# Kernel optimization log

Hardware: AMD Instinct MI355X
Metric: run time of the kernel (lower is better)

Reference implementation:

```python
import jax, jax.numpy as jnp
import numpy as np

B, S, D, H = 4, 2048, 1024, 16
HD = D // H  # head_dim = 64

def setup_inputs() -> dict:
    key = jax.random.key(0)
    ks = jax.random.split(key, 5)
    scale = 1.0 / np.sqrt(D)
    return {
        "x": jax.random.normal(ks[0], (B, S, D), dtype=jnp.float32),
        "Wqkv": jax.random.normal(ks[1], (D, 3 * D), dtype=jnp.float32) * scale,
        "bqkv": jax.random.normal(ks[2], (3 * D,), dtype=jnp.float32) * 0.01,
        "Wo": jax.random.normal(ks[3], (D, D), dtype=jnp.float32) * scale,
        "bo": jax.random.normal(ks[4], (D,), dtype=jnp.float32) * 0.01,
    }

def reference(x, Wqkv, bqkv, Wo, bo):
    b, s, d = x.shape
    # fused QKV projection: [B,S,3D]
    qkv = jnp.einsum("bsd,de->bse", x, Wqkv) + bqkv
    # [B,S,H,3*HD] -> [B,H,S,3*HD], then chunk into q,k,v per head
    qkv = qkv.reshape(b, s, H, 3 * HD).transpose(0, 2, 1, 3)
    q, k, v = jnp.split(qkv, 3, axis=-1)  # each [B,H,S,HD]
    inv_sqrt_dk = jnp.asarray(1.0 / np.sqrt(HD), dtype=x.dtype)
    scores = jnp.einsum("bhqd,bhkd->bhqk", q, k) * inv_sqrt_dk
    attn = jax.nn.softmax(scores, axis=-1)
    values = jnp.einsum("bhqk,bhkd->bhqd", attn, v)  # [B,H,S,HD]
    # NOTE: source reshapes [B,H,S,HD] -> [B,S,H*HD] WITHOUT permuting back
    # (a quirk of the original code); replicated faithfully.
    values = values.reshape(b, s, d)
    out = jnp.einsum("bsd,de->bse", values, Wo) + bo
    return out
```

## Files before the change

### kernel.cpp

```cpp
#include <hip/hip_runtime.h>
#include <hip/hip_bf16.h>
#include <cstdint>

static constexpr int Bq  = 4;
static constexpr int Sq  = 2048;
static constexpr int Dq  = 1024;
static constexpr int Hq  = 16;
static constexpr int HDq = 64;
static constexpr int ROWS = Bq * Sq;
static constexpr int QKV_N = 3 * Dq;

typedef __bf16 bf16x8 __attribute__((ext_vector_type(8)));
typedef __bf16 bf16x4 __attribute__((ext_vector_type(4)));
typedef __bf16 bf16x2 __attribute__((ext_vector_type(2)));
typedef float  floatx4 __attribute__((ext_vector_type(4)));
typedef float  floatx16 __attribute__((ext_vector_type(16)));
typedef unsigned int uintx4 __attribute__((ext_vector_type(4)));

#define MFMA16(a, b, c) __builtin_amdgcn_mfma_f32_16x16x32_bf16((a), (b), (c), 0, 0, 0)
#define MFMA32(a, b, c) __builtin_amdgcn_mfma_f32_32x32x16_bf16((a), (b), (c), 0, 0, 0)

#define QSCALE 0.18033688011112042f

__device__ __forceinline__ void async16(const void* g, void* l) {
    __builtin_amdgcn_global_load_lds(
        (const __attribute__((address_space(1))) uint32_t*)g,
        (__attribute__((address_space(3))) uint32_t*)l, 16, 0, 0);
}

__global__ __launch_bounds__(256) void cvt4_kernel(const float4* __restrict__ in,
                                                   bf16x4* __restrict__ out, int n4) {
    int i = blockIdx.x * 256 + threadIdx.x;
    if (i < n4) {
        float4 v = in[i];
        bf16x4 o;
        o[0] = (__bf16)v.x; o[1] = (__bf16)v.y; o[2] = (__bf16)v.z; o[3] = (__bf16)v.w;
        out[i] = o;
    }
}

__global__ __launch_bounds__(256) void tcvt_kernel(const float* __restrict__ in,
                                                   __bf16* __restrict__ out, int K, int N) {
    __shared__ float t[32][33];
    int n0 = blockIdx.x * 32, k0 = blockIdx.y * 32;
    int c = threadIdx.x & 31, r0 = threadIdx.x >> 5;
#pragma unroll
    for (int rr = 0; rr < 32; rr += 8)
        t[r0 + rr][c] = in[(size_t)(k0 + r0 + rr) * N + n0 + c];
    __syncthreads();
#pragma unroll
    for (int rr = 0; rr < 32; rr += 8)
        out[(size_t)(n0 + r0 + rr) * K + k0 + c] = (__bf16)t[c][r0 + rr];
}

template <int MODE>
__global__ __launch_bounds__(256) void gemm_bt_kernel(const __bf16* __restrict__ A,
                                                      const __bf16* __restrict__ BT,
                                                      const float* __restrict__ bias,
                                                      void* __restrict__ Cout,
                                                      __bf16* __restrict__ Vt,
                                                      int M, int N, int K) {
    __shared__ __bf16 As[128 * 32];
    __shared__ __bf16 Bs[128 * 32];

    const int t = threadIdx.x;
    const int lane = t & 63;
    const int wave = t >> 6;
    const int wm = wave & 1, wn = wave >> 1;
    const int l15 = lane & 15;
    const int kg = (lane >> 4) * 8;

    const int m0 = blockIdx.y * 128;
    const int n0 = blockIdx.x * 128;

    const int srow = t >> 2;
    const int scol = (t & 3) * 8;
    const __bf16* ag = A  + (size_t)(m0 + srow) * K + scol;
    const __bf16* bg = BT + (size_t)(n0 + srow) * K + scol;
    __bf16* al = As + t * 8;
    __bf16* bl = Bs + t * 8;

    floatx4 acc[4][4] = {};

    for (int k0 = 0; k0 < K; k0 += 32) {
        __syncthreads();
        async16(ag + k0,                    al);
        async16(ag + (size_t)64 * K + k0,   al + 2048);
        async16(bg + k0,                    bl);
        async16(bg + (size_t)64 * K + k0,   bl + 2048);
        __syncthreads();

        bf16x8 af[4], bfr[4];
#pragma unroll
        for (int mi = 0; mi < 4; ++mi)
            af[mi] = *(const bf16x8*)(As + (wm * 64 + mi * 16 + l15) * 32 + kg);
#pragma unroll
        for (int ni = 0; ni < 4; ++ni)
            bfr[ni] = *(const bf16x8*)(Bs + (wn * 64 + ni * 16 + l15) * 32 + kg);
#pragma unroll
        for (int mi = 0; mi < 4; ++mi)
#pragma unroll
            for (int ni = 0; ni < 4; ++ni)
                acc[mi][ni] = MFMA16(af[mi], bfr[ni], acc[mi][ni]);
    }

    const int r0 = (lane >> 4) * 4;
    const int wn0 = n0 + wn * 64;

    if (MODE == 2 && (wn0 % 192) == 128) {
#pragma unroll
        for (int ni = 0; ni < 4; ++ni) {
            int col = wn0 + ni * 16 + l15;
            float bv = bias[col];
            int h = col / 192;
            int d = col - h * 192 - 128;
#pragma unroll
            for (int mi = 0; mi < 4; ++mi) {
                int row = m0 + wm * 64 + mi * 16 + r0;
                int b = row >> 11, s = row & 2047;
                bf16x4 vv;
#pragma unroll
                for (int i = 0; i < 4; ++i) vv[i] = (__bf16)(acc[mi][ni][i] + bv);
                *(bf16x4*)(Vt + ((size_t)(b * Hq + h) * HDq + d) * Sq + s) = vv;
            }
        }
    } else {
        const float sc = (MODE == 2 && (wn0 % 192) == 0) ? QSCALE : 1.0f;
#pragma unroll
        for (int ni = 0; ni < 4; ++ni) {
            int col = wn0 + ni * 16 + l15;
            float bv = bias[col];
#pragma unroll
            for (int mi = 0; mi < 4; ++mi) {
#pragma unroll
                for (int i = 0; i < 4; ++i) {
                    int row = m0 + wm * 64 + mi * 16 + r0 + i;
                    float v = (acc[mi][ni][i] + bv) * sc;
                    size_t off = (size_t)row * N + col;
                    if (MODE == 1) ((float*)Cout)[off] = v;
                    else           ((__bf16*)Cout)[off] = (__bf16)v;
                }
            }
        }
    }
}

__global__ __launch_bounds__(256, 2) void attn_kernel(const __bf16* __restrict__ qkv,
                                                      const __bf16* __restrict__ Vt,
                                                      __bf16* __restrict__ v2) {
    const int bh = blockIdx.x;
    const int b = bh >> 4, h = bh & 15;
    const int q0 = blockIdx.y * 256;
    const int tid  = threadIdx.x;
    const int lane = tid & 63;
    const int wave = tid >> 6;
    const int l31  = lane & 31;
    const int hi   = lane >> 5;
    const int kx   = l31 & 7;
    const size_t rs = QKV_N;
    const __bf16* base  = qkv + (size_t)b * Sq * rs + (size_t)h * (3 * HDq);
    const __bf16* vbase = Vt + (size_t)bh * HDq * Sq;

    __shared__ alignas(16) __bf16 Ks[2][64][64];
    __shared__ alignas(16) __bf16 Vs[2][64][64];

    bf16x8 qb[2][4];
#pragma unroll
    for (int qg = 0; qg < 2; ++qg) {
        const __bf16* qr = base + (size_t)(q0 + wave * 64 + qg * 32 + l31) * rs + hi * 8;
#pragma unroll
        for (int st = 0; st < 4; ++st) qb[qg][st] = *(const bf16x8*)(qr + st * 16);
    }

    const int rA = wave * 8 + (lane >> 3);
    const int rB = rA + 32;
    const int sw = ((lane & 7) ^ (rA & 7)) * 8;
    const __bf16* gK0 = base + HDq + (size_t)rA * rs + sw;
    const __bf16* gK1 = base + HDq + (size_t)rB * rs + sw;
    const __bf16* gV0 = vbase + (size_t)rA * Sq + sw;
    const __bf16* gV1 = vbase + (size_t)rB * Sq + sw;
    const int loff0 = wave * 512 + lane * 8;
    const int loff1 = (4 + wave) * 512 + lane * 8;

    auto STAGE = [&](int bufi, int kt) {
        const size_t ko = (size_t)kt * rs;
        async16(gK0 + ko, &Ks[bufi][0][0] + loff0);
        async16(gK1 + ko, &Ks[bufi][0][0] + loff1);
        async16(gV0 + kt, &Vs[bufi][0][0] + loff0);
        async16(gV1 + kt, &Vs[bufi][0][0] + loff1);
    };

    auto softmax_pb = [&](const floatx16& c, float& la, bf16x8* pb) {
        unsigned int W[8];
        float s0 = 0.f, s1 = 0.f;
#pragma unroll
        for (int m = 0; m < 8; ++m) {
            float e0 = __builtin_amdgcn_exp2f(c[2 * m]);
            float e1 = __builtin_amdgcn_exp2f(c[2 * m + 1]);
            s0 += e0; s1 += e1;
            union { bf16x2 v; unsigned int u; } pk;
            pk.v[0] = (__bf16)e0; pk.v[1] = (__bf16)e1;
            W[m] = pk.u;
        }
        la += s0 + s1;
#pragma unroll
        for (int ks = 0; ks < 2; ++ks) {
            auto r0 = __builtin_amdgcn_permlane32_swap(W[ks * 4 + 0], W[ks * 4 + 2], false, false);
            auto r1 = __builtin_amdgcn_permlane32_swap(W[ks * 4 + 1], W[ks * 4 + 3], false, false);
            uintx4 bb; bb[0] = r0[0]; bb[1] = r1[0]; bb[2] = r0[1]; bb[3] = r1[1];
            pb[ks] = __builtin_bit_cast(bf16x8, bb);
        }
    };

    floatx16 o[2][2] = {};
    float la0 = 0.f, la1 = 0.f;

    STAGE(0, 0);
    __syncthreads();

    int cur = 0;
    for (int kt = 0; kt < Sq; kt += 64, cur ^= 1) {
        if (kt + 64 < Sq) STAGE(cur ^ 1, kt + 64);

#pragma unroll
        for (int half = 0; half < 2; ++half) {
            const int key = half * 32 + l31;

            floatx16 c0 = {}, c1 = {};
#pragma unroll
            for (int st = 0; st < 4; ++st) {
                bf16x8 a = *(const bf16x8*)(&Ks[cur][key][((st * 2 + hi) ^ kx) * 8]);
                c0 = MFMA32(a, qb[0][st], c0);
                c1 = MFMA32(a, qb[1][st], c1);
            }

            bf16x8 pb0[2], pb1[2];
            softmax_pb(c0, la0, pb0);
            softmax_pb(c1, la1, pb1);

#pragma unroll
            for (int ks = 0; ks < 2; ++ks) {
                const int kslot = half * 4 + ks * 2 + hi;
                bf16x8 va0 = *(const bf16x8*)(&Vs[cur][l31][(kslot ^ kx) * 8]);
                bf16x8 va1 = *(const bf16x8*)(&Vs[cur][32 + l31][(kslot ^ kx) * 8]);
                o[0][0] = MFMA32(va0, pb0[ks], o[0][0]);
                o[0][1] = MFMA32(va1, pb0[ks], o[0][1]);
                o[1][0] = MFMA32(va0, pb1[ks], o[1][0]);
                o[1][1] = MFMA32(va1, pb1[ks], o[1][1]);
            }
        }
        __syncthreads();
    }

#pragma unroll
    for (int qg = 0; qg < 2; ++qg) {
        float lsum = qg ? la1 : la0;
        float l = lsum + __shfl_xor(lsum, 32);
        float rinv = 1.0f / l;
        const int q = q0 + wave * 64 + qg * 32 + l31;
        size_t row = (size_t)b * Sq + h * 128 + (q >> 4);
        __bf16* vrow = v2 + row * Dq + (size_t)(q & 15) * 64;
#pragma unroll
        for (int gg = 0; gg < 4; ++gg) {
            bf16x4 ov;
#pragma unroll
            for (int i = 0; i < 4; ++i) ov[i] = (__bf16)(o[qg][0][gg * 4 + i] * rinv);
            *(bf16x4*)(vrow + gg * 8 + hi * 4) = ov;
#pragma unroll
            for (int i = 0; i < 4; ++i) ov[i] = (__bf16)(o[qg][1][gg * 4 + i] * rinv);
            *(bf16x4*)(vrow + 32 + gg * 8 + hi * 4) = ov;
        }
    }
}

extern "C" void kernel_launch(void* const* d_in, const int* in_sizes, int n_in,
                              void* d_out, int out_size, void* d_ws, size_t ws_size,
                              hipStream_t stream) {
    const float* x    = (const float*)d_in[0];
    const float* Wqkv = (const float*)d_in[1];
    const float* bqkv = (const float*)d_in[2];
    const float* Wo   = (const float*)d_in[3];
    const float* bo   = (const float*)d_in[4];
    float* out = (float*)d_out;

    __bf16* xb    = (__bf16*)d_ws;
    __bf16* WqkvT = xb    + (size_t)ROWS * Dq;
    __bf16* WoT   = WqkvT + (size_t)QKV_N * Dq;
    __bf16* qkvb  = WoT   + (size_t)Dq * Dq;
    __bf16* Vt    = qkvb  + (size_t)ROWS * QKV_N;
    __bf16* v2    = xb;

    const int nx4 = ROWS * Dq / 4;
    cvt4_kernel<<<(nx4 + 255) / 256, 256, 0, stream>>>((const float4*)x, (bf16x4*)xb, nx4);
    tcvt_kernel<<<dim3(QKV_N / 32, Dq / 32), 256, 0, stream>>>(Wqkv, WqkvT, Dq, QKV_N);
    tcvt_kernel<<<dim3(Dq / 32, Dq / 32), 256, 0, stream>>>(Wo, WoT, Dq, Dq);

    gemm_bt_kernel<2><<<dim3(QKV_N / 128, ROWS / 128), 256, 0, stream>>>(
        xb, WqkvT, bqkv, (void*)qkvb, Vt, ROWS, QKV_N, Dq);

    attn_kernel<<<dim3(Bq * Hq, Sq / 256), 256, 0, stream>>>(qkvb, Vt, v2);

    gemm_bt_kernel<1><<<dim3(Dq / 128, ROWS / 128), 256, 0, stream>>>(
        v2, WoT, bo, (void*)out, nullptr, ROWS, Dq, Dq);
}
```

Baseline: 278.6 us.

## Add dedicated 256x256 QKV GEMM with async double-buffered LDS pipeline

Replaces the generic 128x128 QKV projection GEMM with a specialized 512-thread kernel. It uses 256x256 tiles, 32x32x16 MFMA, XOR-swizzled LDS, async global-to-LDS loads double-buffered across K steps, and interleaves loads with compute phases using barriers and setprio. The goal is higher MFMA utilization and better latency hiding for the largest GEMM. The generic kernel is reduced to the output-projection path only. Costs include larger LDS and register use, and a hand-tuned vmcnt schedule that is fragile.

After: 282.5 us. Within noise of the previous version (+1.4%).

```diff
diff --git a/kernel.cpp b/kernel.cpp
--- a/kernel.cpp
+++ b/kernel.cpp
@@ -51,6 +51,158 @@
 #pragma unroll
     for (int rr = 0; rr < 32; rr += 8)
         out[(size_t)(n0 + r0 + rr) * K + k0 + c] = (__bf16)t[c][r0 + rr];
+}
+
+__global__ __launch_bounds__(512, 2) void gemm_qkv_kernel(const __bf16* __restrict__ A,
+                                                          const __bf16* __restrict__ BT,
+                                                          const float* __restrict__ bias,
+                                                          __bf16* __restrict__ qkvb,
+                                                          __bf16* __restrict__ Vt) {
+    __shared__ __bf16 lds[2][2][2][128][64];
+
+    const int tid  = threadIdx.x;
+    const int lane = tid & 63;
+    const int wave = tid >> 6;
+    const int wm = wave >> 2;
+    const int wn = wave & 3;
+    const int l31 = lane & 31;
+    const int hi  = lane >> 5;
+    const int kx  = l31 & 7;
+
+    const int m0 = blockIdx.y * 256;
+    const int n0 = blockIdx.x * 256;
+
+    const int srow = lane >> 3;
+    const int ssl  = ((lane & 7) ^ srow) * 8;
+    const __bf16* gA = A  + (size_t)(m0 + wave * 16 + srow) * 1024 + ssl;
+    const __bf16* gB = BT + (size_t)(n0 + wave * 16 + srow) * 1024 + ssl;
+
+    auto STAGE = [&](int buf, int op, int half, int ktel) {
+        const __bf16* g = (op ? gB : gA) + (size_t)half * (128 * 1024) + ktel;
+        __bf16* l = &lds[buf][op][half][0][0] + wave * 1024 + lane * 8;
+        async16(g, l);
+        async16(g + 8 * 1024, l + 512);
+    };
+
+    floatx16 acc[4][2] = {};
+
+    STAGE(0, 1, 0, 0);
+    STAGE(0, 0, 0, 0);
+    STAGE(0, 1, 1, 0);
+    STAGE(0, 0, 1, 0);
+    STAGE(1, 1, 0, 64);
+    STAGE(1, 0, 0, 64);
+    asm volatile("s_waitcnt vmcnt(4)" ::: "memory");
+    __builtin_amdgcn_sched_barrier(0);
+    __builtin_amdgcn_s_barrier();
+
+    const int brow = (wn & 1) * 64;
+
+    for (int t = 0; t < 16; ++t) {
+        const int d = t & 1;
+        const __bf16* As = &lds[d][0][wm][0][0];
+        const __bf16* Bs = &lds[d][1][wn >> 1][0][0];
+
+        bf16x8 af[2][4], bf0[4], bf1[4];
+
+#pragma unroll
+        for (int mf = 0; mf < 2; ++mf)
+#pragma unroll
+            for (int ks = 0; ks < 4; ++ks)
+                af[mf][ks] = *(const bf16x8*)(As + (mf * 32 + l31) * 64 + ((ks * 2 + hi) ^ kx) * 8);
+#pragma unroll
+        for (int ks = 0; ks < 4; ++ks)
+            bf0[ks] = *(const bf16x8*)(Bs + (brow + l31) * 64 + ((ks * 2 + hi) ^ kx) * 8);
+        if (t + 1 < 16) STAGE(d ^ 1, 1, 1, (t + 1) * 64);
+        __builtin_amdgcn_s_barrier();
+        __builtin_amdgcn_s_setprio(1);
+#pragma unroll
+        for (int ks = 0; ks < 4; ++ks) {
+            acc[0][0] = MFMA32(af[0][ks], bf0[ks], acc[0][0]);
+            acc[1][0] = MFMA32(af[1][ks], bf0[ks], acc[1][0]);
+        }
+        __builtin_amdgcn_s_setprio(0);
+        __builtin_amdgcn_s_barrier();
+
+#pragma unroll
+        for (int ks = 0; ks < 4; ++ks)
+            bf1[ks] = *(const bf16x8*)(Bs + (brow + 32 + l31) * 64 + ((ks * 2 + hi) ^ kx) * 8);
+        if (t + 1 < 16) STAGE(d ^ 1, 0, 1, (t + 1) * 64);
+        __builtin_amdgcn_s_barrier();
+        __builtin_amdgcn_s_setprio(1);
+#pragma unroll
+        for (int ks = 0; ks < 4; ++ks) {
+            acc[0][1] = MFMA32(af[0][ks], bf1[ks], acc[0][1]);
+            acc[1][1] = MFMA32(af[1][ks], bf1[ks], acc[1][1]);
+        }
+        __builtin_amdgcn_s_setprio(0);
+        __builtin_amdgcn_s_barrier();
+
+#pragma unroll
+        for (int mf = 0; mf < 2; ++mf)
+#pragma unroll
+            for (int ks = 0; ks < 4; ++ks)
+                af[mf][ks] = *(const bf16x8*)(As + ((2 + mf) * 32 + l31) * 64 + ((ks * 2 + hi) ^ kx) * 8);
+        if (t + 2 < 16) STAGE(d, 1, 0, (t + 2) * 64);
+        __builtin_amdgcn_s_barrier();
+        __builtin_amdgcn_s_setprio(1);
+#pragma unroll
+        for (int ks = 0; ks < 4; ++ks) {
+            acc[2][1] = MFMA32(af[0][ks], bf1[ks], acc[2][1]);
+            acc[3][1] = MFMA32(af[1][ks], bf1[ks], acc[3][1]);
+        }
+        __builtin_amdgcn_s_setprio(0);
+        __builtin_amdgcn_s_barrier();
+
+        if (t + 2 < 16) STAGE(d, 0, 0, (t + 2) * 64);
+        __builtin_amdgcn_s_barrier();
+        __builtin_amdgcn_s_setprio(1);
+#pragma unroll
+        for (int ks = 0; ks < 4; ++ks) {
+            acc[2][0] = MFMA32(af[0][ks], bf0[ks], acc[2][0]);
+            acc[3][0] = MFMA32(af[1][ks], bf0[ks], acc[3][0]);
+        }
+        __builtin_amdgcn_s_setprio(0);
+        if (t < 14) {
+            asm volatile("s_waitcnt vmcnt(4)" ::: "memory");
+        } else {
+            asm volatile("s_waitcnt vmcnt(0)" ::: "memory");
+        }
+        __builtin_amdgcn_sched_barrier(0);
+        __builtin_amdgcn_s_barrier();
+    }
+
+#pragma unroll
+    for (int fn = 0; fn < 2; ++fn) {
+        const int cg = n0 + wn * 64 + fn * 32;
+        const int cm = cg % 192;
+        const float bv = bias[cg + l31];
+        if (cm >= 128) {
+            const int hh = cg / 192;
+            const int dd = cm - 128 + l31;
+            const int bb = m0 >> 11;
+            const int sb = (m0 + wm * 128) & 2047;
+            __bf16* vt = Vt + ((size_t)(bb * Hq + hh) * HDq + dd) * Sq + sb;
+#pragma unroll
+            for (int fm = 0; fm < 4; ++fm)
+#pragma unroll
+                for (int g = 0; g < 4; ++g) {
+                    bf16x4 vv;
+#pragma unroll
+                    for (int i = 0; i < 4; ++i) vv[i] = (__bf16)(acc[fm][fn][g * 4 + i] + bv);
+                    *(bf16x4*)(vt + fm * 32 + g * 8 + hi * 4) = vv;
+                }
+        } else {
+            const float sc = (cm < 64) ? QSCALE : 1.0f;
+#pragma unroll
+            for (int fm = 0; fm < 4; ++fm)
+#pragma unroll
+                for (int r = 0; r < 16; ++r) {
+                    int m = m0 + wm * 128 + fm * 32 + (r & 3) + 8 * (r >> 2) + 4 * hi;
+                    qkvb[(size_t)m * QKV_N + cg + l31] = (__bf16)((acc[fm][fn][r] + bv) * sc);
+                }
+        }
+    }
 }
 
 template <int MODE>
@@ -107,39 +259,18 @@
     const int r0 = (lane >> 4) * 4;
     const int wn0 = n0 + wn * 64;
 
-    if (MODE == 2 && (wn0 % 192) == 128) {
-#pragma unroll
-        for (int ni = 0; ni < 4; ++ni) {
-            int col = wn0 + ni * 16 + l15;
-            float bv = bias[col];
-            int h = col / 192;
-            int d = col - h * 192 - 128;
-#pragma unroll
-            for (int mi = 0; mi < 4; ++mi) {
-                int row = m0 + wm * 64 + mi * 16 + r0;
-                int b = row >> 11, s = row & 2047;
-                bf16x4 vv;
-#pragma unroll
-                for (int i = 0; i < 4; ++i) vv[i] = (__bf16)(acc[mi][ni][i] + bv);
-                *(bf16x4*)(Vt + ((size_t)(b * Hq + h) * HDq + d) * Sq + s) = vv;
-            }
-        }
-    } else {
-        const float sc = (MODE == 2 && (wn0 % 192) == 0) ? QSCALE : 1.0f;
-#pragma unroll
-        for (int ni = 0; ni < 4; ++ni) {
-            int col = wn0 + ni * 16 + l15;
-            float bv = bias[col];
-#pragma unroll
-            for (int mi = 0; mi < 4; ++mi) {
-#pragma unroll
-                for (int i = 0; i < 4; ++i) {
-                    int row = m0 + wm * 64 + mi * 16 + r0 + i;
-                    float v = (acc[mi][ni][i] + bv) * sc;
-                    size_t off = (size_t)row * N + col;
-                    if (MODE == 1) ((float*)Cout)[off] = v;
-                    else           ((__bf16*)Cout)[off] = (__bf16)v;
-                }
+#pragma unroll
+    for (int ni = 0; ni < 4; ++ni) {
+        int col = wn0 + ni * 16 + l15;
+        float bv = bias[col];
+#pragma unroll
+        for (int mi = 0; mi < 4; ++mi) {
+#pragma unroll
+            for (int i = 0; i < 4; ++i) {
+                int row = m0 + wm * 64 + mi * 16 + r0 + i;
+                float v = acc[mi][ni][i] + bv;
+                size_t off = (size_t)row * N + col;
+                ((float*)Cout)[off] = v;
             }
         }
     }
@@ -295,8 +426,8 @@
     tcvt_kernel<<<dim3(QKV_N / 32, Dq / 32), 256, 0, stream>>>(Wqkv, WqkvT, Dq, QKV_N);
     tcvt_kernel<<<dim3(Dq / 32, Dq / 32), 256, 0, stream>>>(Wo, WoT, Dq, Dq);
 
-    gemm_bt_kernel<2><<<dim3(QKV_N / 128, ROWS / 128), 256, 0, stream>>>(
-        xb, WqkvT, bqkv, (void*)qkvb, Vt, ROWS, QKV_N, Dq);
+    gemm_qkv_kernel<<<dim3(QKV_N / 256, ROWS / 256), 512, 0, stream>>>(
+        xb, WqkvT, bqkv, qkvb, Vt);
 
     attn_kernel<<<dim3(Bq * Hq, Sq / 256), 256, 0, stream>>>(qkvb, Vt, v2);
 
```
